# Performance work log

Measured on AMD Instinct MI355X. Metric: run time of the kernel, lower is better.

## Reference

```python
import jax, jax.numpy as jnp
import numpy as np

N = 50_000          # nodes
E = 1_600_000       # edges (avg degree 32)
F_IN = 8            # num_static_node_features
F_OUT = 12          # num_timesteps_in (TGCN hidden)
PERIODS = 6         # num_timesteps_out


def setup_inputs() -> dict:
    key = jax.random.key(0)
    ks = jax.random.split(key, 12)
    def n(k, shape, s=0.2):
        return jax.random.normal(k, shape, jnp.float32) * s
    return {
        "x": jax.random.normal(ks[0], (N, F_IN, PERIODS), jnp.float32),
        "edge_index": jax.random.randint(ks[1], (2, E), 0, N, dtype=jnp.int32),
        "edge_weight": jax.random.uniform(ks[2], (E,), jnp.float32),
        "att": n(ks[3], (PERIODS,), 1.0),
        "Wz": n(ks[4], (F_IN, F_OUT)), "bz": jnp.zeros((F_OUT,), jnp.float32),
        "Wr": n(ks[5], (F_IN, F_OUT)), "br": jnp.zeros((F_OUT,), jnp.float32),
        "Wh": n(ks[6], (F_IN, F_OUT)), "bh": jnp.zeros((F_OUT,), jnp.float32),
        "lzW": n(ks[7], (F_OUT, 2 * F_OUT)), "lzb": jnp.zeros((F_OUT,), jnp.float32),
        "lrW": n(ks[8], (F_OUT, 2 * F_OUT)), "lrb": jnp.zeros((F_OUT,), jnp.float32),
        "lhW": n(ks[9], (F_OUT, 2 * F_OUT)), "lhb": jnp.zeros((F_OUT,), jnp.float32),
        "linW": n(ks[10], (PERIODS, F_OUT)), "linb": jnp.zeros((PERIODS,), jnp.float32),
    }


def _gcn_norm(edge_index, edge_weight):
    # PyG gcn_norm: add self loops (weight 1.0), symmetric D^-1/2 A D^-1/2,
    # degree computed from dst (col) of edge_weight.
    src, dst = edge_index[0], edge_index[1]
    loop = jnp.arange(N, dtype=src.dtype)
    src = jnp.concatenate([src, loop])
    dst = jnp.concatenate([dst, loop])
    ew = jnp.concatenate([edge_weight, jnp.ones((N,), edge_weight.dtype)])
    deg = jax.ops.segment_sum(ew, dst, num_segments=N)
    dinv = jnp.where(deg > 0, 1.0 / jnp.sqrt(deg), 0.0)
    return src, dst, dinv[src] * ew * dinv[dst]


def _gcn_conv(xp, W, b, src, dst, norm):
    h = xp @ W                                  # [N, F_OUT]
    msg = norm[:, None] * h[src]                # gather over edges
    return jax.ops.segment_sum(msg, dst, num_segments=N) + b


def reference(x, edge_index, edge_weight, att, Wz, bz, Wr, br, Wh, bh,
              lzW, lzb, lrW, lrb, lhW, lhb, linW, linb):
    src, dst, norm = _gcn_norm(edge_index, edge_weight)
    H0 = jnp.zeros((N, F_OUT), x.dtype)  # A3TGCN passes H=None each period

    def tgcn_cell(xp):  # xp: [N, F_IN]
        Z = jax.nn.sigmoid(
            jnp.concatenate([_gcn_conv(xp, Wz, bz, src, dst, norm), H0], -1) @ lzW.T + lzb)
        R = jax.nn.sigmoid(
            jnp.concatenate([_gcn_conv(xp, Wr, br, src, dst, norm), H0], -1) @ lrW.T + lrb)
        Ht = jnp.tanh(
            jnp.concatenate([_gcn_conv(xp, Wh, bh, src, dst, norm), H0 * R], -1) @ lhW.T + lhb)
        return Z * H0 + (1.0 - Z) * Ht

    probs = jax.nn.softmax(att)                  # [P]
    Hs = jax.vmap(tgcn_cell, in_axes=2)(x)       # [P, N, F_OUT]
    H = jnp.einsum('p,pnf->nf', probs, Hs)       # attention-weighted sum
    h = jax.nn.relu(H)
    return h @ linW.T + linb                     # [N, PERIODS]
```

## Files before the change

### kernel.cpp

```cpp
#include <hip/hip_runtime.h>
#include <hip/hip_fp16.h>

#define N_NODES 50000
#define N_EDGES 1600000
#define F_IN 8
#define F_OUT 12
#define PERIODS 6
#define FP 48
#define BKT_SH 7
#define BKT_N 128
#define NBKT ((N_NODES + BKT_N - 1) / BKT_N)
#define CHK 4096
#define NCHK ((N_EDGES + CHK - 1) / CHK)
#define SEG_CAP 4736

__global__ void k_zero(unsigned int* __restrict__ cursor) {
    int i = threadIdx.x;
    if (i < NBKT) cursor[i] = 0u;
}

__global__ void __launch_bounds__(512) k_scatter(const int4* __restrict__ src4,
                                                 const int4* __restrict__ dst4,
                                                 const float4* __restrict__ ew4,
                                                 unsigned int* __restrict__ cursor,
                                                 unsigned long long* __restrict__ part) {
    __shared__ unsigned int h[NBKT];
    __shared__ unsigned int gbase[NBKT];
    int tid = threadIdx.x, blk = blockIdx.x;
    for (int k = tid; k < NBKT; k += 512) h[k] = 0u;
    __syncthreads();
    int qbase = blk * (CHK / 4);
    int bv[8]; unsigned int lr[8], lo[8], hiw[8]; bool val[8];
    #pragma unroll
    for (int u = 0; u < 2; u++) {
        int q = qbase + u * 512 + tid;
        bool v = (q < N_EDGES / 4);
        int4 ss = v ? src4[q] : make_int4(0, 0, 0, 0);
        int4 dd = v ? dst4[q] : make_int4(0, 0, 0, 0);
        float4 ww = v ? ew4[q] : make_float4(0.f, 0.f, 0.f, 0.f);
        int s[4] = { ss.x, ss.y, ss.z, ss.w };
        int d[4] = { dd.x, dd.y, dd.z, dd.w };
        float w[4] = { ww.x, ww.y, ww.z, ww.w };
        #pragma unroll
        for (int e = 0; e < 4; e++) {
            int i = u * 4 + e;
            val[i] = v;
            if (v) {
                int b = d[e] >> BKT_SH;
                bv[i] = b;
                lr[i] = atomicAdd(&h[b], 1u);
                lo[i] = ((unsigned int)(d[e] & (BKT_N - 1)) << 24) | (unsigned int)s[e];
                hiw[i] = __float_as_uint(w[e]);
            }
        }
    }
    __syncthreads();
    for (int k = tid; k < NBKT; k += 512) {
        unsigned int c = h[k];
        gbase[k] = c ? atomicAdd(&cursor[k], c) : 0u;
    }
    __syncthreads();
    #pragma unroll
    for (int i = 0; i < 8; i++) {
        if (!val[i]) continue;
        unsigned int off = gbase[bv[i]] + lr[i];
        if (off < SEG_CAP)
            part[(size_t)bv[i] * SEG_CAP + off] =
                ((unsigned long long)hiw[i] << 32) | lo[i];
    }
}

__global__ void __launch_bounds__(512) k_bucket(const unsigned long long* __restrict__ part,
                                                const unsigned int* __restrict__ cursor,
                                                const float* __restrict__ x,
                                                int2* __restrict__ offs2,
                                                float* __restrict__ dinv_g,
                                                uint4* __restrict__ xs,
                                                unsigned int* __restrict__ csr4) {
    __shared__ uint2 stage[SEG_CAP];
    __shared__ unsigned int cnt[BKT_N], rowstart[BKT_N], sc[BKT_N];
    __shared__ float degf[BKT_N], dinv_l[BKT_N];
    int tid = threadIdx.x, k = blockIdx.x;
    unsigned int base = (unsigned int)k * SEG_CAP;
    unsigned int m = cursor[k];
    if (m > SEG_CAP) m = SEG_CAP;
    if (tid < BKT_N) { cnt[tid] = 0u; degf[tid] = 1.0f; }
    __syncthreads();

    for (unsigned int i = tid; i < m; i += 512) {
        unsigned long long p = __builtin_nontemporal_load(&part[base + i]);
        unsigned int lo = (unsigned int)p;
        unsigned int hi = (unsigned int)(p >> 32);
        unsigned int j = (lo >> 24) & (BKT_N - 1);
        unsigned int r = atomicAdd(&cnt[j], 1u);
        atomicAdd(&degf[j], __uint_as_float(hi));
        if (r > 255u) r = 255u;
        stage[i] = make_uint2(lo | (r << 16), hi);
    }
    __syncthreads();

    if (tid < 64) {
        unsigned int a = cnt[tid], b = cnt[tid + 64];
        unsigned int sa = a;
        #pragma unroll
        for (int off = 1; off < 64; off <<= 1) {
            unsigned int tv = __shfl_up(sa, off);
            if ((tid & 63) >= off) sa += tv;
        }
        unsigned int tot = __shfl(sa, 63);
        unsigned int sb = b;
        #pragma unroll
        for (int off = 1; off < 64; off <<= 1) {
            unsigned int tv = __shfl_up(sb, off);
            if ((tid & 63) >= off) sb += tv;
        }
        sc[tid] = sa;
        sc[tid + 64] = sb + tot;
    }
    __syncthreads();

    int n0 = k * BKT_N;
    int nn = N_NODES - n0; if (nn > BKT_N) nn = BKT_N;

    if (tid < BKT_N) {
        unsigned int rs = sc[tid] - cnt[tid];
        rowstart[tid] = rs;
        float dv = rsqrtf(degf[tid]);
        dinv_l[tid] = dv;
        if (tid < nn) {
            dinv_g[n0 + tid] = dv;
            offs2[n0 + tid] = make_int2((int)(base + rs), (int)(base + sc[tid]));
        }
    }
    __syncthreads();

    for (unsigned int i = tid; i < m; i += 512) {
        uint2 vv = stage[i];
        unsigned int j = (vv.x >> 24) & (BKT_N - 1);
        unsigned int r = (vv.x >> 16) & 0xFFu;
        __half hw = __float2half(__uint_as_float(vv.y));
        unsigned int entry = ((unsigned int)__half_as_ushort(hw) << 16) |
                             (vv.x & 0xFFFFu);
        csr4[base + rowstart[j] + r] = entry;
    }

    for (int idx = tid; idx < nn * 6; idx += 512) {
        int j = idx / 6, c = idx % 6;
        float di = dinv_l[j];
        const float4* xr = (const float4*)(x + (size_t)(n0 + j) * FP + c * 8);
        float4 a = xr[0], b = xr[1];
        __half2 h0 = __floats2half2_rn(di * a.x, di * a.y);
        __half2 h1 = __floats2half2_rn(di * a.z, di * a.w);
        __half2 h2 = __floats2half2_rn(di * b.x, di * b.y);
        __half2 h3 = __floats2half2_rn(di * b.z, di * b.w);
        uint4 o;
        o.x = *(unsigned int*)&h0; o.y = *(unsigned int*)&h1;
        o.z = *(unsigned int*)&h2; o.w = *(unsigned int*)&h3;
        xs[(size_t)(n0 + j) * 6 + c] = o;
    }
}

__global__ void __launch_bounds__(192) k_gnode(const uint4* __restrict__ xs,
                                               const float* __restrict__ dinv,
                                               const int2* __restrict__ offs2,
                                               const unsigned int* __restrict__ csr4,
                                               const float* __restrict__ att,
                                               const float* __restrict__ Wz,
                                               const float* __restrict__ bz,
                                               const float* __restrict__ Wh,
                                               const float* __restrict__ bh,
                                               const float* __restrict__ lzW,
                                               const float* __restrict__ lzb,
                                               const float* __restrict__ lhW,
                                               const float* __restrict__ lhb,
                                               const float* __restrict__ linW,
                                               const float* __restrict__ linb,
                                               float* __restrict__ out) {
    __shared__ float row[8][48];
    __shared__ float gzs[8][72];
    __shared__ float ghs[8][72];
    __shared__ float Hl[8][12];

    int tid = threadIdx.x;
    int L = tid / 24, r = tid % 24, c = r >> 2, g = r & 3;
    int n = blockIdx.x * 8 + L;

    int2 oe = offs2[n];
    const unsigned int* rowp = csr4 + oe.x;
    int cnt = oe.y - oe.x;
    float a0 = 0.f, a1 = 0.f, a2 = 0.f, a3 = 0.f;
    float a4 = 0.f, a5 = 0.f, a6 = 0.f, a7 = 0.f;
    int kk = 0;
    for (; kk + 16 <= cnt; kk += 16) {
        unsigned int p[4]; uint4 v[4];
        #pragma unroll
        for (int u = 0; u < 4; u++)
            p[u] = __builtin_nontemporal_load(rowp + kk + 4 * u + g);
        #pragma unroll
        for (int u = 0; u < 4; u++)
            v[u] = xs[(size_t)(p[u] & 0xFFFFu) * 6 + c];
        #pragma unroll
        for (int u = 0; u < 4; u++) {
            float w = __half2float(__ushort_as_half((unsigned short)(p[u] >> 16)));
            float2 e0 = __half22float2(*(__half2*)&v[u].x);
            float2 e1 = __half22float2(*(__half2*)&v[u].y);
            float2 e2 = __half22float2(*(__half2*)&v[u].z);
            float2 e3 = __half22float2(*(__half2*)&v[u].w);
            a0 += w * e0.x; a1 += w * e0.y; a2 += w * e1.x; a3 += w * e1.y;
            a4 += w * e2.x; a5 += w * e2.y; a6 += w * e3.x; a7 += w * e3.y;
        }
    }
    for (int jj = kk + g; jj < cnt; jj += 4) {
        unsigned int p = __builtin_nontemporal_load(rowp + jj);
        float w = __half2float(__ushort_as_half((unsigned short)(p >> 16)));
        uint4 v = xs[(size_t)(p & 0xFFFFu) * 6 + c];
        float2 e0 = __half22float2(*(__half2*)&v.x);
        float2 e1 = __half22float2(*(__half2*)&v.y);
        float2 e2 = __half22float2(*(__half2*)&v.z);
        float2 e3 = __half22float2(*(__half2*)&v.w);
        a0 += w * e0.x; a1 += w * e0.y; a2 += w * e1.x; a3 += w * e1.y;
        a4 += w * e2.x; a5 += w * e2.y; a6 += w * e3.x; a7 += w * e3.y;
    }
    a0 += __shfl_xor(a0, 1); a1 += __shfl_xor(a1, 1);
    a2 += __shfl_xor(a2, 1); a3 += __shfl_xor(a3, 1);
    a4 += __shfl_xor(a4, 1); a5 += __shfl_xor(a5, 1);
    a6 += __shfl_xor(a6, 1); a7 += __shfl_xor(a7, 1);
    a0 += __shfl_xor(a0, 2); a1 += __shfl_xor(a1, 2);
    a2 += __shfl_xor(a2, 2); a3 += __shfl_xor(a3, 2);
    a4 += __shfl_xor(a4, 2); a5 += __shfl_xor(a5, 2);
    a6 += __shfl_xor(a6, 2); a7 += __shfl_xor(a7, 2);
    if (g == 0) {
        uint4 sf = xs[(size_t)n * 6 + c];
        float2 s0 = __half22float2(*(__half2*)&sf.x);
        float2 s1 = __half22float2(*(__half2*)&sf.y);
        float2 s2 = __half22float2(*(__half2*)&sf.z);
        float2 s3 = __half22float2(*(__half2*)&sf.w);
        float di = dinv[n];
        row[L][8 * c + 0] = di * (a0 + s0.x); row[L][8 * c + 1] = di * (a1 + s0.y);
        row[L][8 * c + 2] = di * (a2 + s1.x); row[L][8 * c + 3] = di * (a3 + s1.y);
        row[L][8 * c + 4] = di * (a4 + s2.x); row[L][8 * c + 5] = di * (a5 + s2.y);
        row[L][8 * c + 6] = di * (a6 + s3.x); row[L][8 * c + 7] = di * (a7 + s3.y);
    }
    __syncthreads();

    for (int it = r; it < 72; it += 24) {
        int p = it / 12, q = it - p * 12;
        float gz = bz[q], gh = bh[q];
        #pragma unroll
        for (int f = 0; f < F_IN; f++) {
            float xv = row[L][f * 6 + p];
            gz += xv * Wz[f * F_OUT + q];
            gh += xv * Wh[f * F_OUT + q];
        }
        gzs[L][it] = gz; ghs[L][it] = gh;
    }
    __syncthreads();

    if (r < 12) {
        float a[PERIODS];
        float mx = -1e30f;
        #pragma unroll
        for (int p = 0; p < PERIODS; p++) { a[p] = att[p]; mx = fmaxf(mx, a[p]); }
        float se = 0.f;
        #pragma unroll
        for (int p = 0; p < PERIODS; p++) { a[p] = __expf(a[p] - mx); se += a[p]; }
        float inv = 1.f / se;
        int j = r;
        float hacc = 0.f;
        #pragma unroll
        for (int p = 0; p < PERIODS; p++) {
            float z = lzb[j], t2 = lhb[j];
            #pragma unroll
            for (int q = 0; q < F_OUT; q++) {
                z  += gzs[L][p * 12 + q] * lzW[j * (2 * F_OUT) + q];
                t2 += ghs[L][p * 12 + q] * lhW[j * (2 * F_OUT) + q];
            }
            float Z = 1.f / (1.f + __expf(-z));
            float e2 = __expf(2.f * t2);
            float th = 1.f - __fdividef(2.f, e2 + 1.f);
            hacc += (a[p] * inv) * (1.f - Z) * th;
        }
        Hl[L][j] = fmaxf(hacc, 0.f);
    }
    __syncthreads();

    if (r < PERIODS) {
        float acc = linb[r];
        #pragma unroll
        for (int j = 0; j < F_OUT; j++)
            acc += Hl[L][j] * linW[r * F_OUT + j];
        out[(size_t)n * PERIODS + r] = acc;
    }
}

extern "C" void kernel_launch(void* const* d_in, const int* in_sizes, int n_in,
                              void* d_out, int out_size, void* d_ws, size_t ws_size,
                              hipStream_t stream) {
    const float* x    = (const float*)d_in[0];
    const int*   ei   = (const int*)d_in[1];
    const float* ew   = (const float*)d_in[2];
    const float* att  = (const float*)d_in[3];
    const float* Wz   = (const float*)d_in[4];
    const float* bz   = (const float*)d_in[5];
    const float* Wh   = (const float*)d_in[8];
    const float* bh   = (const float*)d_in[9];
    const float* lzW  = (const float*)d_in[10];
    const float* lzb  = (const float*)d_in[11];
    const float* lhW  = (const float*)d_in[14];
    const float* lhb  = (const float*)d_in[15];
    const float* linW = (const float*)d_in[16];
    const float* linb = (const float*)d_in[17];
    float* out = (float*)d_out;

    uint4* xs   = (uint4*)d_ws;
    unsigned long long* part = (unsigned long long*)(xs + (size_t)N_NODES * 6);
    unsigned int* csr4 = (unsigned int*)(part + (size_t)NBKT * SEG_CAP);
    int2*  offs2 = (int2*)(csr4 + (size_t)NBKT * SEG_CAP);
    float* dinv  = (float*)(offs2 + N_NODES);
    unsigned int* cursor = (unsigned int*)(dinv + N_NODES);

    const int* srcp = ei;
    const int* dstp = ei + N_EDGES;

    k_zero<<<1, 512, 0, stream>>>(cursor);
    k_scatter<<<NCHK, 512, 0, stream>>>((const int4*)srcp, (const int4*)dstp,
                                        (const float4*)ew, cursor, part);
    k_bucket<<<NBKT, 512, 0, stream>>>(part, cursor, x, offs2, dinv, xs, csr4);
    k_gnode<<<N_NODES / 8, 192, 0, stream>>>(xs, dinv, offs2, csr4, att,
                                             Wz, bz, Wh, bh, lzW, lzb, lhW, lhb,
                                             linW, linb, out);
}
```

Measured before the change: 187.0 us.

## Replace bucketed CSR build with XCC-partitioned direct per-node scatter into fixed-stride rows

The two-pass bucket scatter plus per-bucket local sort is replaced by a single scatter kernel. It writes each edge directly into a fixed-capacity per-node row (stride 96) using global per-node atomics for the cursor and degree. Destination ranges are split into 8 partitions, and each XCC starts on its own partition through a dynamic chunk ticket, so the atomics and writes for a node range tend to stay in one XCC's L2. Every block re-reads the whole edge list once per partition (8 passes), issues many global atomics, and silently drops any edges past degree 96.

After: 475.3 us. 2.54x slower.

```diff
diff --git a/kernel.cpp b/kernel.cpp
--- a/kernel.cpp
+++ b/kernel.cpp
@@ -7,162 +7,88 @@
 #define F_OUT 12
 #define PERIODS 6
 #define FP 48
-#define BKT_SH 7
-#define BKT_N 128
-#define NBKT ((N_NODES + BKT_N - 1) / BKT_N)
-#define CHK 4096
-#define NCHK ((N_EDGES + CHK - 1) / CHK)
-#define SEG_CAP 4736
-
-__global__ void k_zero(unsigned int* __restrict__ cursor) {
-    int i = threadIdx.x;
-    if (i < NBKT) cursor[i] = 0u;
-}
-
-__global__ void __launch_bounds__(512) k_scatter(const int4* __restrict__ src4,
-                                                 const int4* __restrict__ dst4,
-                                                 const float4* __restrict__ ew4,
-                                                 unsigned int* __restrict__ cursor,
-                                                 unsigned long long* __restrict__ part) {
-    __shared__ unsigned int h[NBKT];
-    __shared__ unsigned int gbase[NBKT];
-    int tid = threadIdx.x, blk = blockIdx.x;
-    for (int k = tid; k < NBKT; k += 512) h[k] = 0u;
-    __syncthreads();
-    int qbase = blk * (CHK / 4);
-    int bv[8]; unsigned int lr[8], lo[8], hiw[8]; bool val[8];
-    #pragma unroll
-    for (int u = 0; u < 2; u++) {
-        int q = qbase + u * 512 + tid;
-        bool v = (q < N_EDGES / 4);
-        int4 ss = v ? src4[q] : make_int4(0, 0, 0, 0);
-        int4 dd = v ? dst4[q] : make_int4(0, 0, 0, 0);
-        float4 ww = v ? ew4[q] : make_float4(0.f, 0.f, 0.f, 0.f);
-        int s[4] = { ss.x, ss.y, ss.z, ss.w };
-        int d[4] = { dd.x, dd.y, dd.z, dd.w };
-        float w[4] = { ww.x, ww.y, ww.z, ww.w };
-        #pragma unroll
-        for (int e = 0; e < 4; e++) {
-            int i = u * 4 + e;
-            val[i] = v;
-            if (v) {
-                int b = d[e] >> BKT_SH;
-                bv[i] = b;
-                lr[i] = atomicAdd(&h[b], 1u);
-                lo[i] = ((unsigned int)(d[e] & (BKT_N - 1)) << 24) | (unsigned int)s[e];
-                hiw[i] = __float_as_uint(w[e]);
+#define DEG_CAP 96
+#define NPART 8
+#define PART_N (N_NODES / NPART)
+#define CE 6400
+#define NCHUNK (N_EDGES / CE)
+#define DSCAT_BLOCKS 2048
+
+__device__ __forceinline__ unsigned int xcc_id() {
+    unsigned int x;
+    asm volatile("s_getreg_b32 %0, hwreg(HW_REG_XCC_ID)" : "=s"(x));
+    return x & 7u;
+}
+
+__global__ void k_init(unsigned int* __restrict__ cursor, float* __restrict__ deg,
+                       unsigned int* __restrict__ ticket) {
+    int t = blockIdx.x * blockDim.x + threadIdx.x;
+    if (t < N_NODES) { cursor[t] = 0u; deg[t] = 1.0f; }
+    if (t < NPART) ticket[t] = 0u;
+}
+
+__global__ void __launch_bounds__(256) k_dscat(const int* __restrict__ src,
+                                               const int* __restrict__ dst,
+                                               const float* __restrict__ ew,
+                                               unsigned int* __restrict__ cursor,
+                                               float* __restrict__ deg,
+                                               unsigned int* __restrict__ csr4,
+                                               unsigned int* __restrict__ ticket) {
+    __shared__ unsigned int ts;
+    unsigned int my = xcc_id();
+    for (int po = 0; po < NPART; ++po) {
+        unsigned int p = (my + po) & (NPART - 1);
+        int nlo = (int)p * PART_N, nhi = nlo + PART_N;
+        while (true) {
+            if (threadIdx.x == 0) ts = atomicAdd(&ticket[p], 1u);
+            __syncthreads();
+            unsigned int t = ts;
+            __syncthreads();
+            if (t >= NCHUNK) break;
+            int base = (int)t * CE;
+            for (int i = threadIdx.x; i < CE; i += 256) {
+                int e = base + i;
+                int d = dst[e];
+                if (d >= nlo && d < nhi) {
+                    int s = src[e];
+                    float w = ew[e];
+                    unsigned int pos = atomicAdd(&cursor[d], 1u);
+                    atomicAdd(&deg[d], w);
+                    if (pos < DEG_CAP) {
+                        __half hw = __float2half(w);
+                        csr4[(size_t)d * DEG_CAP + pos] =
+                            ((unsigned int)__half_as_ushort(hw) << 16) | (unsigned int)s;
+                    }
+                }
             }
         }
     }
-    __syncthreads();
-    for (int k = tid; k < NBKT; k += 512) {
-        unsigned int c = h[k];
-        gbase[k] = c ? atomicAdd(&cursor[k], c) : 0u;
-    }
-    __syncthreads();
-    #pragma unroll
-    for (int i = 0; i < 8; i++) {
-        if (!val[i]) continue;
-        unsigned int off = gbase[bv[i]] + lr[i];
-        if (off < SEG_CAP)
-            part[(size_t)bv[i] * SEG_CAP + off] =
-                ((unsigned long long)hiw[i] << 32) | lo[i];
-    }
-}
-
-__global__ void __launch_bounds__(512) k_bucket(const unsigned long long* __restrict__ part,
-                                                const unsigned int* __restrict__ cursor,
-                                                const float* __restrict__ x,
-                                                int2* __restrict__ offs2,
-                                                float* __restrict__ dinv_g,
-                                                uint4* __restrict__ xs,
-                                                unsigned int* __restrict__ csr4) {
-    __shared__ uint2 stage[SEG_CAP];
-    __shared__ unsigned int cnt[BKT_N], rowstart[BKT_N], sc[BKT_N];
-    __shared__ float degf[BKT_N], dinv_l[BKT_N];
-    int tid = threadIdx.x, k = blockIdx.x;
-    unsigned int base = (unsigned int)k * SEG_CAP;
-    unsigned int m = cursor[k];
-    if (m > SEG_CAP) m = SEG_CAP;
-    if (tid < BKT_N) { cnt[tid] = 0u; degf[tid] = 1.0f; }
-    __syncthreads();
-
-    for (unsigned int i = tid; i < m; i += 512) {
-        unsigned long long p = __builtin_nontemporal_load(&part[base + i]);
-        unsigned int lo = (unsigned int)p;
-        unsigned int hi = (unsigned int)(p >> 32);
-        unsigned int j = (lo >> 24) & (BKT_N - 1);
-        unsigned int r = atomicAdd(&cnt[j], 1u);
-        atomicAdd(&degf[j], __uint_as_float(hi));
-        if (r > 255u) r = 255u;
-        stage[i] = make_uint2(lo | (r << 16), hi);
-    }
-    __syncthreads();
-
-    if (tid < 64) {
-        unsigned int a = cnt[tid], b = cnt[tid + 64];
-        unsigned int sa = a;
-        #pragma unroll
-        for (int off = 1; off < 64; off <<= 1) {
-            unsigned int tv = __shfl_up(sa, off);
-            if ((tid & 63) >= off) sa += tv;
-        }
-        unsigned int tot = __shfl(sa, 63);
-        unsigned int sb = b;
-        #pragma unroll
-        for (int off = 1; off < 64; off <<= 1) {
-            unsigned int tv = __shfl_up(sb, off);
-            if ((tid & 63) >= off) sb += tv;
-        }
-        sc[tid] = sa;
-        sc[tid + 64] = sb + tot;
-    }
-    __syncthreads();
-
-    int n0 = k * BKT_N;
-    int nn = N_NODES - n0; if (nn > BKT_N) nn = BKT_N;
-
-    if (tid < BKT_N) {
-        unsigned int rs = sc[tid] - cnt[tid];
-        rowstart[tid] = rs;
-        float dv = rsqrtf(degf[tid]);
-        dinv_l[tid] = dv;
-        if (tid < nn) {
-            dinv_g[n0 + tid] = dv;
-            offs2[n0 + tid] = make_int2((int)(base + rs), (int)(base + sc[tid]));
-        }
-    }
-    __syncthreads();
-
-    for (unsigned int i = tid; i < m; i += 512) {
-        uint2 vv = stage[i];
-        unsigned int j = (vv.x >> 24) & (BKT_N - 1);
-        unsigned int r = (vv.x >> 16) & 0xFFu;
-        __half hw = __float2half(__uint_as_float(vv.y));
-        unsigned int entry = ((unsigned int)__half_as_ushort(hw) << 16) |
-                             (vv.x & 0xFFFFu);
-        csr4[base + rowstart[j] + r] = entry;
-    }
-
-    for (int idx = tid; idx < nn * 6; idx += 512) {
-        int j = idx / 6, c = idx % 6;
-        float di = dinv_l[j];
-        const float4* xr = (const float4*)(x + (size_t)(n0 + j) * FP + c * 8);
-        float4 a = xr[0], b = xr[1];
-        __half2 h0 = __floats2half2_rn(di * a.x, di * a.y);
-        __half2 h1 = __floats2half2_rn(di * a.z, di * a.w);
-        __half2 h2 = __floats2half2_rn(di * b.x, di * b.y);
-        __half2 h3 = __floats2half2_rn(di * b.z, di * b.w);
-        uint4 o;
-        o.x = *(unsigned int*)&h0; o.y = *(unsigned int*)&h1;
-        o.z = *(unsigned int*)&h2; o.w = *(unsigned int*)&h3;
-        xs[(size_t)(n0 + j) * 6 + c] = o;
-    }
+}
+
+__global__ void __launch_bounds__(256) k_xs(const float* __restrict__ x,
+                                            const float* __restrict__ deg,
+                                            float* __restrict__ dinv,
+                                            uint4* __restrict__ xs) {
+    int t = blockIdx.x * 256 + threadIdx.x;
+    if (t >= N_NODES * 6) return;
+    int n = t / 6, c = t % 6;
+    float di = rsqrtf(deg[n]);
+    if (c == 0) dinv[n] = di;
+    const float4* xr = (const float4*)(x + (size_t)n * FP + c * 8);
+    float4 a = xr[0], b = xr[1];
+    __half2 h0 = __floats2half2_rn(di * a.x, di * a.y);
+    __half2 h1 = __floats2half2_rn(di * a.z, di * a.w);
+    __half2 h2 = __floats2half2_rn(di * b.x, di * b.y);
+    __half2 h3 = __floats2half2_rn(di * b.z, di * b.w);
+    uint4 o;
+    o.x = *(unsigned int*)&h0; o.y = *(unsigned int*)&h1;
+    o.z = *(unsigned int*)&h2; o.w = *(unsigned int*)&h3;
+    xs[t] = o;
 }
 
 __global__ void __launch_bounds__(192) k_gnode(const uint4* __restrict__ xs,
                                                const float* __restrict__ dinv,
-                                               const int2* __restrict__ offs2,
+                                               const unsigned int* __restrict__ cursor,
                                                const unsigned int* __restrict__ csr4,
                                                const float* __restrict__ att,
                                                const float* __restrict__ Wz,
@@ -185,9 +111,9 @@
     int L = tid / 24, r = tid % 24, c = r >> 2, g = r & 3;
     int n = blockIdx.x * 8 + L;
 
-    int2 oe = offs2[n];
-    const unsigned int* rowp = csr4 + oe.x;
-    int cnt = oe.y - oe.x;
+    int cnt = (int)cursor[n];
+    if (cnt > DEG_CAP) cnt = DEG_CAP;
+    const unsigned int* rowp = csr4 + (size_t)n * DEG_CAP;
     float a0 = 0.f, a1 = 0.f, a2 = 0.f, a3 = 0.f;
     float a4 = 0.f, a5 = 0.f, a6 = 0.f, a7 = 0.f;
     int kk = 0;
@@ -313,20 +239,19 @@
     float* out = (float*)d_out;
 
     uint4* xs   = (uint4*)d_ws;
-    unsigned long long* part = (unsigned long long*)(xs + (size_t)N_NODES * 6);
-    unsigned int* csr4 = (unsigned int*)(part + (size_t)NBKT * SEG_CAP);
-    int2*  offs2 = (int2*)(csr4 + (size_t)NBKT * SEG_CAP);
-    float* dinv  = (float*)(offs2 + N_NODES);
-    unsigned int* cursor = (unsigned int*)(dinv + N_NODES);
+    unsigned int* csr4 = (unsigned int*)(xs + (size_t)N_NODES * 6);
+    unsigned int* cursor = csr4 + (size_t)N_NODES * DEG_CAP;
+    float* deg  = (float*)(cursor + N_NODES);
+    float* dinv = deg + N_NODES;
+    unsigned int* ticket = (unsigned int*)(dinv + N_NODES);
 
     const int* srcp = ei;
     const int* dstp = ei + N_EDGES;
 
-    k_zero<<<1, 512, 0, stream>>>(cursor);
-    k_scatter<<<NCHK, 512, 0, stream>>>((const int4*)srcp, (const int4*)dstp,
-                                        (const float4*)ew, cursor, part);
-    k_bucket<<<NBKT, 512, 0, stream>>>(part, cursor, x, offs2, dinv, xs, csr4);
-    k_gnode<<<N_NODES / 8, 192, 0, stream>>>(xs, dinv, offs2, csr4, att,
+    k_init<<<(N_NODES + 511) / 512, 512, 0, stream>>>(cursor, deg, ticket);
+    k_dscat<<<DSCAT_BLOCKS, 256, 0, stream>>>(srcp, dstp, ew, cursor, deg, csr4, ticket);
+    k_xs<<<(N_NODES * 6 + 255) / 256, 256, 0, stream>>>(x, deg, dinv, xs);
+    k_gnode<<<N_NODES / 8, 192, 0, stream>>>(xs, dinv, cursor, csr4, att,
                                              Wz, bz, Wh, bh, lzW, lzb, lhW, lhb,
                                              linW, linb, out);
 }
```

## Pad CSR rows to multiples of four and vectorize neighbor index loads

Applied to the files above, without the earlier changes.

Each node's CSR row start is padded to a 4-entry boundary, and buckets get a larger aligned stride. This lets each lane in the gather kernel load four contiguous neighbor entries with one 16-byte nontemporal load, where it previously issued four strided scalar loads. The tail loop is changed so each lane handles a contiguous group of four. The scatter and bucket kernels also move from 512 to 1024 threads per block, one int4 per thread, which changes per-thread work and occupancy. Padding adds some memory and uninitialized pad slots, but those slots are never read because row end is start plus count.

Result: no change. 187.3 us (+0.1%).

```diff
diff --git a/kernel.cpp b/kernel.cpp
--- a/kernel.cpp
+++ b/kernel.cpp
@@ -13,81 +13,80 @@
 #define CHK 4096
 #define NCHK ((N_EDGES + CHK - 1) / CHK)
 #define SEG_CAP 4736
+#define SEG_AL  5120
+
+typedef unsigned int u32x4 __attribute__((ext_vector_type(4)));
 
 __global__ void k_zero(unsigned int* __restrict__ cursor) {
     int i = threadIdx.x;
     if (i < NBKT) cursor[i] = 0u;
 }
 
-__global__ void __launch_bounds__(512) k_scatter(const int4* __restrict__ src4,
-                                                 const int4* __restrict__ dst4,
-                                                 const float4* __restrict__ ew4,
-                                                 unsigned int* __restrict__ cursor,
-                                                 unsigned long long* __restrict__ part) {
+__global__ void __launch_bounds__(1024) k_scatter(const int4* __restrict__ src4,
+                                                  const int4* __restrict__ dst4,
+                                                  const float4* __restrict__ ew4,
+                                                  unsigned int* __restrict__ cursor,
+                                                  unsigned long long* __restrict__ part) {
     __shared__ unsigned int h[NBKT];
     __shared__ unsigned int gbase[NBKT];
     int tid = threadIdx.x, blk = blockIdx.x;
-    for (int k = tid; k < NBKT; k += 512) h[k] = 0u;
-    __syncthreads();
-    int qbase = blk * (CHK / 4);
-    int bv[8]; unsigned int lr[8], lo[8], hiw[8]; bool val[8];
+    for (int k = tid; k < NBKT; k += 1024) h[k] = 0u;
+    __syncthreads();
+    int q = blk * 1024 + tid;
+    bool v = (q < N_EDGES / 4);
+    int4 ss = v ? src4[q] : make_int4(0, 0, 0, 0);
+    int4 dd = v ? dst4[q] : make_int4(0, 0, 0, 0);
+    float4 ww = v ? ew4[q] : make_float4(0.f, 0.f, 0.f, 0.f);
+    int s[4] = { ss.x, ss.y, ss.z, ss.w };
+    int d[4] = { dd.x, dd.y, dd.z, dd.w };
+    float w[4] = { ww.x, ww.y, ww.z, ww.w };
+    int bv[4]; unsigned int lr[4], lo[4], hiw[4];
     #pragma unroll
-    for (int u = 0; u < 2; u++) {
-        int q = qbase + u * 512 + tid;
-        bool v = (q < N_EDGES / 4);
-        int4 ss = v ? src4[q] : make_int4(0, 0, 0, 0);
-        int4 dd = v ? dst4[q] : make_int4(0, 0, 0, 0);
-        float4 ww = v ? ew4[q] : make_float4(0.f, 0.f, 0.f, 0.f);
-        int s[4] = { ss.x, ss.y, ss.z, ss.w };
-        int d[4] = { dd.x, dd.y, dd.z, dd.w };
-        float w[4] = { ww.x, ww.y, ww.z, ww.w };
-        #pragma unroll
-        for (int e = 0; e < 4; e++) {
-            int i = u * 4 + e;
-            val[i] = v;
-            if (v) {
-                int b = d[e] >> BKT_SH;
-                bv[i] = b;
-                lr[i] = atomicAdd(&h[b], 1u);
-                lo[i] = ((unsigned int)(d[e] & (BKT_N - 1)) << 24) | (unsigned int)s[e];
-                hiw[i] = __float_as_uint(w[e]);
-            }
-        }
-    }
-    __syncthreads();
-    for (int k = tid; k < NBKT; k += 512) {
+    for (int e = 0; e < 4; e++) {
+        if (v) {
+            int b = d[e] >> BKT_SH;
+            bv[e] = b;
+            lr[e] = atomicAdd(&h[b], 1u);
+            lo[e] = ((unsigned int)(d[e] & (BKT_N - 1)) << 24) | (unsigned int)s[e];
+            hiw[e] = __float_as_uint(w[e]);
+        }
+    }
+    __syncthreads();
+    for (int k = tid; k < NBKT; k += 1024) {
         unsigned int c = h[k];
         gbase[k] = c ? atomicAdd(&cursor[k], c) : 0u;
     }
     __syncthreads();
-    #pragma unroll
-    for (int i = 0; i < 8; i++) {
-        if (!val[i]) continue;
-        unsigned int off = gbase[bv[i]] + lr[i];
-        if (off < SEG_CAP)
-            part[(size_t)bv[i] * SEG_CAP + off] =
-                ((unsigned long long)hiw[i] << 32) | lo[i];
-    }
-}
-
-__global__ void __launch_bounds__(512) k_bucket(const unsigned long long* __restrict__ part,
-                                                const unsigned int* __restrict__ cursor,
-                                                const float* __restrict__ x,
-                                                int2* __restrict__ offs2,
-                                                float* __restrict__ dinv_g,
-                                                uint4* __restrict__ xs,
-                                                unsigned int* __restrict__ csr4) {
+    if (v) {
+        #pragma unroll
+        for (int e = 0; e < 4; e++) {
+            unsigned int off = gbase[bv[e]] + lr[e];
+            if (off < SEG_CAP)
+                part[(size_t)bv[e] * SEG_CAP + off] =
+                    ((unsigned long long)hiw[e] << 32) | lo[e];
+        }
+    }
+}
+
+__global__ void __launch_bounds__(1024) k_bucket(const unsigned long long* __restrict__ part,
+                                                 const unsigned int* __restrict__ cursor,
+                                                 const float* __restrict__ x,
+                                                 int2* __restrict__ offs2,
+                                                 float* __restrict__ dinv_g,
+                                                 uint4* __restrict__ xs,
+                                                 unsigned int* __restrict__ csr4) {
     __shared__ uint2 stage[SEG_CAP];
     __shared__ unsigned int cnt[BKT_N], rowstart[BKT_N], sc[BKT_N];
     __shared__ float degf[BKT_N], dinv_l[BKT_N];
     int tid = threadIdx.x, k = blockIdx.x;
     unsigned int base = (unsigned int)k * SEG_CAP;
+    unsigned int cbase = (unsigned int)k * SEG_AL;
     unsigned int m = cursor[k];
     if (m > SEG_CAP) m = SEG_CAP;
     if (tid < BKT_N) { cnt[tid] = 0u; degf[tid] = 1.0f; }
     __syncthreads();
 
-    for (unsigned int i = tid; i < m; i += 512) {
+    for (unsigned int i = tid; i < m; i += 1024) {
         unsigned long long p = __builtin_nontemporal_load(&part[base + i]);
         unsigned int lo = (unsigned int)p;
         unsigned int hi = (unsigned int)(p >> 32);
@@ -100,7 +99,8 @@
     __syncthreads();
 
     if (tid < 64) {
-        unsigned int a = cnt[tid], b = cnt[tid + 64];
+        unsigned int a = (cnt[tid] + 3u) & ~3u;
+        unsigned int b = (cnt[tid + 64] + 3u) & ~3u;
         unsigned int sa = a;
         #pragma unroll
         for (int off = 1; off < 64; off <<= 1) {
@@ -123,28 +123,30 @@
     int nn = N_NODES - n0; if (nn > BKT_N) nn = BKT_N;
 
     if (tid < BKT_N) {
-        unsigned int rs = sc[tid] - cnt[tid];
+        unsigned int ca = (cnt[tid] + 3u) & ~3u;
+        unsigned int rs = sc[tid] - ca;
         rowstart[tid] = rs;
         float dv = rsqrtf(degf[tid]);
         dinv_l[tid] = dv;
         if (tid < nn) {
             dinv_g[n0 + tid] = dv;
-            offs2[n0 + tid] = make_int2((int)(base + rs), (int)(base + sc[tid]));
-        }
-    }
-    __syncthreads();
-
-    for (unsigned int i = tid; i < m; i += 512) {
+            offs2[n0 + tid] = make_int2((int)(cbase + rs),
+                                        (int)(cbase + rs + cnt[tid]));
+        }
+    }
+    __syncthreads();
+
+    for (unsigned int i = tid; i < m; i += 1024) {
         uint2 vv = stage[i];
         unsigned int j = (vv.x >> 24) & (BKT_N - 1);
         unsigned int r = (vv.x >> 16) & 0xFFu;
         __half hw = __float2half(__uint_as_float(vv.y));
         unsigned int entry = ((unsigned int)__half_as_ushort(hw) << 16) |
                              (vv.x & 0xFFFFu);
-        csr4[base + rowstart[j] + r] = entry;
-    }
-
-    for (int idx = tid; idx < nn * 6; idx += 512) {
+        csr4[cbase + rowstart[j] + r] = entry;
+    }
+
+    for (int idx = tid; idx < nn * 6; idx += 1024) {
         int j = idx / 6, c = idx % 6;
         float di = dinv_l[j];
         const float4* xr = (const float4*)(x + (size_t)(n0 + j) * FP + c * 8);
@@ -192,10 +194,9 @@
     float a4 = 0.f, a5 = 0.f, a6 = 0.f, a7 = 0.f;
     int kk = 0;
     for (; kk + 16 <= cnt; kk += 16) {
-        unsigned int p[4]; uint4 v[4];
-        #pragma unroll
-        for (int u = 0; u < 4; u++)
-            p[u] = __builtin_nontemporal_load(rowp + kk + 4 * u + g);
+        u32x4 pc = __builtin_nontemporal_load((const u32x4*)(rowp + kk + 4 * g));
+        unsigned int p[4] = { pc.x, pc.y, pc.z, pc.w };
+        uint4 v[4];
         #pragma unroll
         for (int u = 0; u < 4; u++)
             v[u] = xs[(size_t)(p[u] & 0xFFFFu) * 6 + c];
@@ -210,7 +211,8 @@
             a4 += w * e2.x; a5 += w * e2.y; a6 += w * e3.x; a7 += w * e3.y;
         }
     }
-    for (int jj = kk + g; jj < cnt; jj += 4) {
+    int tlo = kk + 4 * g, thi = tlo + 4; if (thi > cnt) thi = cnt;
+    for (int jj = tlo; jj < thi; jj++) {
         unsigned int p = __builtin_nontemporal_load(rowp + jj);
         float w = __half2float(__ushort_as_half((unsigned short)(p >> 16)));
         uint4 v = xs[(size_t)(p & 0xFFFFu) * 6 + c];
@@ -315,7 +317,7 @@
     uint4* xs   = (uint4*)d_ws;
     unsigned long long* part = (unsigned long long*)(xs + (size_t)N_NODES * 6);
     unsigned int* csr4 = (unsigned int*)(part + (size_t)NBKT * SEG_CAP);
-    int2*  offs2 = (int2*)(csr4 + (size_t)NBKT * SEG_CAP);
+    int2*  offs2 = (int2*)(csr4 + (size_t)NBKT * SEG_AL);
     float* dinv  = (float*)(offs2 + N_NODES);
     unsigned int* cursor = (unsigned int*)(dinv + N_NODES);
 
@@ -323,9 +325,9 @@
     const int* dstp = ei + N_EDGES;
 
     k_zero<<<1, 512, 0, stream>>>(cursor);
-    k_scatter<<<NCHK, 512, 0, stream>>>((const int4*)srcp, (const int4*)dstp,
-                                        (const float4*)ew, cursor, part);
-    k_bucket<<<NBKT, 512, 0, stream>>>(part, cursor, x, offs2, dinv, xs, csr4);
+    k_scatter<<<NCHK, 1024, 0, stream>>>((const int4*)srcp, (const int4*)dstp,
+                                         (const float4*)ew, cursor, part);
+    k_bucket<<<NBKT, 1024, 0, stream>>>(part, cursor, x, offs2, dinv, xs, csr4);
     k_gnode<<<N_NODES / 8, 192, 0, stream>>>(xs, dinv, offs2, csr4, att,
                                              Wz, bz, Wh, bh, lzW, lzb, lhW, lhb,
                                              linW, linb, out);
```
